# Performance work log

Hardware: AMD Instinct MI355X
Metric: run time of the kernel (lower is better)

Reference implementation:

```python
import jax, jax.numpy as jnp
import numpy as np

NUM_NODES = 1024
NUM_HEADS = 8
HIDDEN = 256
BOND_DIM = 64
NUM_LAYERS = 3


def _build_edge_index(n):
    # ring + chord graph, both directions -> 4n directed edges, no duplicate (src,tgt) pairs
    u = np.arange(n)
    src = np.concatenate([u, u, (u + 1) % n, (u + 2) % n])
    dst = np.concatenate([(u + 1) % n, (u + 2) % n, u, u])
    return jnp.asarray(np.stack([src, dst]), dtype=jnp.int32)


def setup_inputs() -> dict:
    key = jax.random.key(0)
    ks = jax.random.split(key, 16)
    H, L, B = HIDDEN, NUM_LAYERS, BOND_DIM
    E = 4 * NUM_NODES
    s = 0.02
    inp = {
        "edge_index": _build_edge_index(NUM_NODES),
        "bond_features": jax.random.normal(ks[0], (E, B), jnp.float32),
        # bond_embedding Linear + W_h Linear (stored as [in, out])
        "W_emb": jax.random.normal(ks[1], (B, H), jnp.float32) * s,
        "b_emb": jnp.zeros((H,), jnp.float32),
        "W_h": jax.random.normal(ks[2], (H, H), jnp.float32) * s,
        "b_h": jnp.zeros((H,), jnp.float32),
        # per-layer attention block: pre-LN, qkv in-proj, out-proj
        "ln1_g": jnp.ones((L, H), jnp.float32),
        "ln1_b": jnp.zeros((L, H), jnp.float32),
        "in_w": jax.random.normal(ks[3], (L, H, 3 * H), jnp.float32) * s,
        "in_b": jnp.zeros((L, 3 * H), jnp.float32),
        "out_w": jax.random.normal(ks[4], (L, H, H), jnp.float32) * s,
        "out_b": jnp.zeros((L, H), jnp.float32),
        # per-layer bond_update: Linear -> LayerNorm -> GELU
        "up_w": jax.random.normal(ks[5], (L, H, H), jnp.float32) * s,
        "up_b": jnp.zeros((L, H), jnp.float32),
        "ln2_g": jnp.ones((L, H), jnp.float32),
        "ln2_b": jnp.zeros((L, H), jnp.float32),
    }
    return inp


def _layer_norm(x, g, b, eps=1e-5):
    m = jnp.mean(x, axis=-1, keepdims=True)
    v = jnp.var(x, axis=-1, keepdims=True)
    return (x - m) * jax.lax.rsqrt(v + eps) * g + b


def _mha(x, in_w, in_b, out_w, out_b):
    # x: [E, H]; standard torch MultiheadAttention (batch of 1)
    E, H = x.shape
    d = H // NUM_HEADS
    qkv = x @ in_w + in_b                                  # [E, 3H]
    q, k, v = jnp.split(qkv, 3, axis=-1)
    q = q.reshape(E, NUM_HEADS, d).transpose(1, 0, 2)       # [h, E, d]
    k = k.reshape(E, NUM_HEADS, d).transpose(1, 0, 2)
    v = v.reshape(E, NUM_HEADS, d).transpose(1, 0, 2)
    scores = jnp.einsum("hqd,hkd->hqk", q, k) / jnp.sqrt(jnp.float32(d))
    p = jax.nn.softmax(scores, axis=-1)
    o = jnp.einsum("hqk,hkd->hqd", p, v)                    # [h, E, d]
    o = o.transpose(1, 0, 2).reshape(E, H)
    return o @ out_w + out_b


def _bond_aggregation(edge_index, h):
    # r_e = sum_{e' : tgt(e')=tgt(e), src(e')!=src(e)} (h[e'] - h[e])
    # with no duplicate (src,tgt) pairs this is S[tgt] - deg[tgt] * h
    tgt = edge_index[1]
    S = jax.ops.segment_sum(h, tgt, num_segments=NUM_NODES)                 # [N, H]
    deg = jax.ops.segment_sum(jnp.ones(h.shape[:1], h.dtype), tgt, num_segments=NUM_NODES)
    return S[tgt] - deg[tgt][:, None] * h


def reference(edge_index, bond_features, W_emb, b_emb, W_h, b_h,
              ln1_g, ln1_b, in_w, in_b, out_w, out_b,
              up_w, up_b, ln2_g, ln2_b):
    h = jax.nn.gelu(bond_features @ W_emb + b_emb, approximate=False)
    h = h @ W_h + b_h
    for t in range(NUM_LAYERS):
        r = _bond_aggregation(edge_index, h)
        xn = _layer_norm(r, ln1_g[t], ln1_b[t])
        attn = _mha(xn, in_w[t], in_b[t], out_w[t], out_b[t])
        # block output = attn + r (residual inside block), forward adds + r again
        t_ij = attn + r + r
        u = t_ij @ up_w[t] + up_b[t]
        h = jax.nn.gelu(_layer_norm(u, ln2_g[t], ln2_b[t]), approximate=False)
    return h
```

## Files before the change

kernel.cpp:

```cpp
#include <hip/hip_runtime.h>
#include <hip/hip_bf16.h>
#include <math.h>

#define N_NODES 1024
#define NE      4096
#define HDIM    256
#define QSCALE  0.2550348634f

typedef __hip_bfloat16 bf16;
typedef __attribute__((ext_vector_type(8))) short bf16x8;
typedef __attribute__((ext_vector_type(4))) float f32x4;

__device__ __forceinline__ float u2f(unsigned short u) {
  return __uint_as_float(((unsigned)u) << 16);
}
__device__ __forceinline__ short f2bs(float x) {
  unsigned u = __float_as_uint(x);
  unsigned r = u + 0x7FFFu + ((u >> 16) & 1u);
  return (short)(r >> 16);
}
__device__ __forceinline__ float gelu_f(float x) {
  return 0.5f * x * (1.0f + erff(x * 0.70710678118654752f));
}
__device__ __forceinline__ short rdbf(const void* p, int i, int flag) {
  return flag ? ((const short*)p)[i] : f2bs(((const float*)p)[i]);
}
__device__ __forceinline__ float fexp2(float x) {
#if __has_builtin(__builtin_amdgcn_exp2f)
  return __builtin_amdgcn_exp2f(x);
#else
  return exp2f(x);
#endif
}
__device__ __forceinline__ unsigned pk2(float lo, float hi) {
  return (__float_as_uint(hi) & 0xFFFF0000u) | (__float_as_uint(lo) >> 16);
}

__global__ __launch_bounds__(64) void k_detect(const unsigned* __restrict__ w,
                                               int* __restrict__ flag) {
  int t = threadIdx.x;
  int cnt = 0;
  for (int i = 0; i < 16; ++i) {
    unsigned v = w[t * 16 + i];
    unsigned e = (v >> 7) & 0xFFu;
    cnt += (e >= 100u && e <= 132u) ? 1 : 0;
  }
#pragma unroll
  for (int k = 1; k < 64; k <<= 1) cnt += __shfl_xor(cnt, k, 64);
  if (t == 0) *flag = (cnt > 512) ? 1 : 0;
}

struct WPtrs { const void* w_emb; const void* w_h; const void* in_w;
               const void* out_w; const void* up_w; };
__global__ __launch_bounds__(256) void k_prep_w(WPtrs a, short* __restrict__ Wt,
                                                const int* __restrict__ flag) {
  int i = blockIdx.x * 256 + threadIdx.x;
  if (i >= 1064960) return;
  const int fl = *flag;
  if (i < 16384) {
    int k = i >> 8, n = i & 255;
    Wt[n * 64 + k] = rdbf(a.w_emb, i, fl);
  } else if (i < 81920) {
    int j = i - 16384;
    int k = j >> 8, n = j & 255;
    Wt[16384 + n * 256 + k] = rdbf(a.w_h, j, fl);
  } else if (i < 671744) {
    int j = i - 81920;
    int t = j / 196608, jj = j % 196608;
    int k = jj / 768, n = jj % 768;
    Wt[81920 + t * 196608 + n * 256 + k] = rdbf(a.in_w, j, fl);
  } else if (i < 868352) {
    int j = i - 671744;
    int t = j >> 16, jj = j & 65535;
    int k = jj >> 8, n = jj & 255;
    Wt[671744 + t * 65536 + n * 256 + k] = rdbf(a.out_w, j, fl);
  } else {
    int j = i - 868352;
    int t = j >> 16, jj = j & 65535;
    int k = jj >> 8, n = jj & 255;
    Wt[868352 + t * 65536 + n * 256 + k] = rdbf(a.up_w, j, fl);
  }
}

struct PPtrs { const void* p[9]; };
__global__ __launch_bounds__(256) void k_cvt_small(PPtrs a, float* __restrict__ dst,
                                                   const int* __restrict__ flag) {
  const int sz[9] = {256, 256, 768, 768, 2304, 768, 768, 768, 768};
  int i = blockIdx.x * 256 + threadIdx.x;
  if (i >= 7424) return;
  int seg = 0, off = i;
  while (off >= sz[seg]) { off -= sz[seg]; ++seg; }
  dst[i] = *flag ? u2f(((const unsigned short*)a.p[seg])[off])
                 : ((const float*)a.p[seg])[off];
}

__global__ __launch_bounds__(256) void k_cvt_bond(const void* __restrict__ src,
                                                  short* __restrict__ dst,
                                                  const int* __restrict__ flag) {
  int i = blockIdx.x * 256 + threadIdx.x;
  if (i < NE * 64) dst[i] = rdbf(src, i, *flag);
}

__global__ __launch_bounds__(256) void k_build_inv(const int* __restrict__ tgt,
                                                   int* __restrict__ cnt,
                                                   int* __restrict__ inv) {
  int e = blockIdx.x * 256 + threadIdx.x;
  if (e < NE) {
    int t = tgt[e];
    int s = atomicAdd(&cnt[t], 1);
    if (s < 8) inv[t * 8 + s] = e;
  }
}

template <bool GELU, bool RES, bool WF, bool WB>
__global__ __launch_bounds__(256) void k_mgemm(const short* __restrict__ A,
                                               const short* __restrict__ Bt,
                                               const float* __restrict__ bias,
                                               const float* __restrict__ res,
                                               float* __restrict__ outF,
                                               short* __restrict__ outB,
                                               int M, int N, int K) {
  __shared__ alignas(16) short As[64 * 40];
  __shared__ alignas(16) short Bs[64 * 40];
  const int tid = threadIdx.x;
  const int wave = tid >> 6, lane = tid & 63;
  const int m = lane & 15, quad = lane >> 4;
  const int bm = blockIdx.x * 64, bn = blockIdx.y * 64;
  const int m0 = (wave & 1) * 32, n0 = (wave >> 1) * 32;
  const int srow = tid >> 2, sko = (tid & 3) * 8;

  f32x4 acc[2][2];
  acc[0][0] = acc[0][1] = acc[1][0] = acc[1][1] = (f32x4){0.f, 0.f, 0.f, 0.f};

  int4 pa = *(const int4*)(A + (size_t)(bm + srow) * K + sko);
  int4 pb = *(const int4*)(Bt + (size_t)(bn + srow) * K + sko);

  for (int k0 = 0; k0 < K; k0 += 32) {
    __syncthreads();
    *(int4*)&As[srow * 40 + sko] = pa;
    *(int4*)&Bs[srow * 40 + sko] = pb;
    __syncthreads();
    if (k0 + 32 < K) {
      pa = *(const int4*)(A + (size_t)(bm + srow) * K + k0 + 32 + sko);
      pb = *(const int4*)(Bt + (size_t)(bn + srow) * K + k0 + 32 + sko);
    }
    bf16x8 a0 = *(const bf16x8*)&As[(m0 + m) * 40 + quad * 8];
    bf16x8 a1 = *(const bf16x8*)&As[(m0 + 16 + m) * 40 + quad * 8];
    bf16x8 b0 = *(const bf16x8*)&Bs[(n0 + m) * 40 + quad * 8];
    bf16x8 b1 = *(const bf16x8*)&Bs[(n0 + 16 + m) * 40 + quad * 8];
    acc[0][0] = __builtin_amdgcn_mfma_f32_16x16x32_bf16(a0, b0, acc[0][0], 0, 0, 0);
    acc[0][1] = __builtin_amdgcn_mfma_f32_16x16x32_bf16(a0, b1, acc[0][1], 0, 0, 0);
    acc[1][0] = __builtin_amdgcn_mfma_f32_16x16x32_bf16(a1, b0, acc[1][0], 0, 0, 0);
    acc[1][1] = __builtin_amdgcn_mfma_f32_16x16x32_bf16(a1, b1, acc[1][1], 0, 0, 0);
  }

#pragma unroll
  for (int i = 0; i < 2; ++i)
#pragma unroll
    for (int j = 0; j < 2; ++j) {
      const int col = bn + n0 + j * 16 + m;
      const float bv = bias[col];
#pragma unroll
      for (int r = 0; r < 4; ++r) {
        const int row = bm + m0 + i * 16 + quad * 4 + r;
        float v = acc[i][j][r] + bv;
        if (GELU) v = gelu_f(v);
        if (RES) v += 2.0f * res[(size_t)row * N + col];
        if (WF) outF[(size_t)row * N + col] = v;
        if (WB) outB[(size_t)row * N + col] = f2bs(v);
      }
    }
}

__global__ __launch_bounds__(256) void k_mgemm_qkv(const short* __restrict__ A,
                                                   const short* __restrict__ Bt,
                                                   const float* __restrict__ bias,
                                                   short* __restrict__ Qh,
                                                   short* __restrict__ Kh,
                                                   short* __restrict__ Vt) {
  const int K = 256;
  __shared__ alignas(16) short As[64 * 40];
  __shared__ alignas(16) short Bs[64 * 40];
  const int tid = threadIdx.x;
  const int wave = tid >> 6, lane = tid & 63;
  const int m = lane & 15, quad = lane >> 4;
  const int bm = blockIdx.x * 64, bn = blockIdx.y * 64;
  const int m0 = (wave & 1) * 32, n0 = (wave >> 1) * 32;
  const int srow = tid >> 2, sko = (tid & 3) * 8;

  f32x4 acc[2][2];
  acc[0][0] = acc[0][1] = acc[1][0] = acc[1][1] = (f32x4){0.f, 0.f, 0.f, 0.f};

  int4 pa = *(const int4*)(A + (size_t)(bm + srow) * K + sko);
  int4 pb = *(const int4*)(Bt + (size_t)(bn + srow) * K + sko);

  for (int k0 = 0; k0 < K; k0 += 32) {
    __syncthreads();
    *(int4*)&As[srow * 40 + sko] = pa;
    *(int4*)&Bs[srow * 40 + sko] = pb;
    __syncthreads();
    if (k0 + 32 < K) {
      pa = *(const int4*)(A + (size_t)(bm + srow) * K + k0 + 32 + sko);
      pb = *(const int4*)(Bt + (size_t)(bn + srow) * K + k0 + 32 + sko);
    }
    bf16x8 a0 = *(const bf16x8*)&As[(m0 + m) * 40 + quad * 8];
    bf16x8 a1 = *(const bf16x8*)&As[(m0 + 16 + m) * 40 + quad * 8];
    bf16x8 b0 = *(const bf16x8*)&Bs[(n0 + m) * 40 + quad * 8];
    bf16x8 b1 = *(const bf16x8*)&Bs[(n0 + 16 + m) * 40 + quad * 8];
    acc[0][0] = __builtin_amdgcn_mfma_f32_16x16x32_bf16(a0, b0, acc[0][0], 0, 0, 0);
    acc[0][1] = __builtin_amdgcn_mfma_f32_16x16x32_bf16(a0, b1, acc[0][1], 0, 0, 0);
    acc[1][0] = __builtin_amdgcn_mfma_f32_16x16x32_bf16(a1, b0, acc[1][0], 0, 0, 0);
    acc[1][1] = __builtin_amdgcn_mfma_f32_16x16x32_bf16(a1, b1, acc[1][1], 0, 0, 0);
  }

#pragma unroll
  for (int i = 0; i < 2; ++i)
#pragma unroll
    for (int j = 0; j < 2; ++j) {
      const int col = bn + n0 + j * 16 + m;
      const float bv = bias[col];
      const int row0 = bm + m0 + i * 16 + quad * 4;
      if (col < 256) {
        const int head = col >> 5, d = col & 31;
#pragma unroll
        for (int r = 0; r < 4; ++r)
          Qh[(size_t)head * 131072 + (row0 + r) * 32 + d] =
              f2bs((acc[i][j][r] + bv) * QSCALE);
      } else if (col < 512) {
        const int c = col - 256, head = c >> 5, d = c & 31;
#pragma unroll
        for (int r = 0; r < 4; ++r)
          Kh[(size_t)head * 131072 + (row0 + r) * 32 + d] = f2bs(acc[i][j][r] + bv);
      } else {
        const int c = col - 512, head = c >> 5, d = c & 31;
        const int p0 = (row0 & ~63) + ((row0 >> 5) & 1) * 32 +
                       ((row0 >> 2) & 3) * 8 + ((row0 >> 4) & 1) * 4;
        ushort4 w;
        w.x = (unsigned short)f2bs(acc[i][j][0] + bv);
        w.y = (unsigned short)f2bs(acc[i][j][1] + bv);
        w.z = (unsigned short)f2bs(acc[i][j][2] + bv);
        w.w = (unsigned short)f2bs(acc[i][j][3] + bv);
        *(ushort4*)(Vt + (size_t)head * 131072 + d * 4096 + p0) = w;
      }
    }
}

__global__ __launch_bounds__(256) void k_rln2(const int* __restrict__ tgt,
                                              const int* __restrict__ cnt,
                                              const int* __restrict__ inv,
                                              const float* __restrict__ h,
                                              const float* __restrict__ g,
                                              const float* __restrict__ b,
                                              float* __restrict__ r,
                                              short* __restrict__ xnb) {
  __shared__ float red1[4], red2[4];
  const int e = blockIdx.x, d = threadIdx.x;
  const int t = tgt[e];
  const int c = cnt[t];
  float S = 0.f;
  for (int j = 0; j < c; ++j)
    S += h[(size_t)inv[t * 8 + j] * HDIM + d];
  float rv = S - (float)c * h[(size_t)e * HDIM + d];
  r[(size_t)e * HDIM + d] = rv;

  float s = rv;
#pragma unroll
  for (int k = 1; k < 64; k <<= 1) s += __shfl_xor(s, k, 64);
  if ((d & 63) == 0) red1[d >> 6] = s;
  __syncthreads();
  float mean = (red1[0] + red1[1] + red1[2] + red1[3]) * (1.0f / HDIM);
  float diff = rv - mean;
  float sq = diff * diff;
#pragma unroll
  for (int k = 1; k < 64; k <<= 1) sq += __shfl_xor(sq, k, 64);
  if ((d & 63) == 0) red2[d >> 6] = sq;
  __syncthreads();
  float var = (red2[0] + red2[1] + red2[2] + red2[3]) * (1.0f / HDIM);
  xnb[(size_t)e * HDIM + d] = f2bs(diff * rsqrtf(var + 1e-5f) * g[d] + b[d]);
}

__global__ __launch_bounds__(256) void k_ln_gelu(const float* __restrict__ u,
                                                 const float* __restrict__ g,
                                                 const float* __restrict__ b,
                                                 float* __restrict__ hout,
                                                 void* __restrict__ finalout,
                                                 const int* __restrict__ flag) {
  __shared__ float red1[4], red2[4];
  const int e = blockIdx.x, d = threadIdx.x;
  float v = u[(size_t)e * HDIM + d];
  float s = v;
#pragma unroll
  for (int k = 1; k < 64; k <<= 1) s += __shfl_xor(s, k, 64);
  if ((d & 63) == 0) red1[d >> 6] = s;
  __syncthreads();
  float mean = (red1[0] + red1[1] + red1[2] + red1[3]) * (1.0f / HDIM);
  float diff = v - mean;
  float sq = diff * diff;
#pragma unroll
  for (int k = 1; k < 64; k <<= 1) sq += __shfl_xor(sq, k, 64);
  if ((d & 63) == 0) red2[d >> 6] = sq;
  __syncthreads();
  float var = (red2[0] + red2[1] + red2[2] + red2[3]) * (1.0f / HDIM);
  float xh = diff * rsqrtf(var + 1e-5f) * g[d] + b[d];
  float out = gelu_f(xh);
  hout[(size_t)e * HDIM + d] = out;
  if (finalout) {
    if (*flag)
      ((bf16*)finalout)[(size_t)e * HDIM + d] = __float2bfloat16(out);
    else
      ((float*)finalout)[(size_t)e * HDIM + d] = out;
  }
}

__global__ __launch_bounds__(256) void k_flash4(const short* __restrict__ Qh,
                                                const short* __restrict__ Kh,
                                                const short* __restrict__ Vt,
                                                short* __restrict__ Opart,
                                                float* __restrict__ lpart) {
  __shared__ alignas(16) short Ks[64 * 40];
  __shared__ alignas(16) short Vs[32 * 70 + 8];
  const int head = blockIdx.y, split = blockIdx.z;
  const int tid = threadIdx.x;
  const int wave = tid >> 6, lane = tid & 63;
  const int m = lane & 15, quad = lane >> 4;
  const int q0 = blockIdx.x * 256 + wave * 64;

  const short* Qb = Qh + (size_t)head * 131072;
  const short* Kb = Kh + (size_t)head * 131072;
  const short* Vb = Vt + (size_t)head * 131072;

  bf16x8 qf[4];
#pragma unroll
  for (int a = 0; a < 4; ++a)
    qf[a] = *(const bf16x8*)(Qb + (q0 + a * 16 + m) * 32 + quad * 8);

  f32x4 O[4][2];
  f32x4 lacc[4];
#pragma unroll
  for (int a = 0; a < 4; ++a) {
    O[a][0] = O[a][1] = (f32x4){0.f, 0.f, 0.f, 0.f};
    lacc[a] = (f32x4){0.f, 0.f, 0.f, 0.f};
  }

  bf16x8 ones;
#pragma unroll
  for (int i = 0; i < 8; ++i) ones[i] = (short)0x3F80;

  const int base = split * 1024;
  const int krow = tid >> 2, ko = (tid & 3) * 8;
  const int vrow = tid >> 3, vo = (tid & 7) * 8;
  const short* kstage = Kb + (size_t)(base + krow) * 32 + ko;
  const short* vstage = Vb + (size_t)vrow * 4096 + base + vo;

  int4 rk = *(const int4*)(kstage);
  int4 rv = *(const int4*)(vstage);

#pragma unroll 1
  for (int kb = 0; kb < 16; ++kb) {
    __syncthreads();
    *(int4*)&Ks[krow * 40 + ko] = rk;
    *(int4*)&Vs[vrow * 70 + vo] = rv;
    __syncthreads();
    if (kb < 15) {
      rk = *(const int4*)(kstage + (kb + 1) * 2048);
      rv = *(const int4*)(vstage + (kb + 1) * 64);
    }

    bf16x8 kc0 = *(const bf16x8*)&Ks[(0 * 16 + m) * 40 + quad * 8];
    bf16x8 kc1 = *(const bf16x8*)&Ks[(1 * 16 + m) * 40 + quad * 8];
    bf16x8 kc2 = *(const bf16x8*)&Ks[(2 * 16 + m) * 40 + quad * 8];
    bf16x8 kc3 = *(const bf16x8*)&Ks[(3 * 16 + m) * 40 + quad * 8];
    bf16x8 vc0 = *(const bf16x8*)&Vs[m * 70 + quad * 8];
    bf16x8 vc1 = *(const bf16x8*)&Vs[(m + 16) * 70 + quad * 8];
    bf16x8 vc2 = *(const bf16x8*)&Vs[m * 70 + 32 + quad * 8];
    bf16x8 vc3 = *(const bf16x8*)&Vs[(m + 16) * 70 + 32 + quad * 8];

    const f32x4 z = {0.f, 0.f, 0.f, 0.f};
#pragma unroll
    for (int a = 0; a < 4; ++a) {
      f32x4 S0 = __builtin_amdgcn_mfma_f32_16x16x32_bf16(kc0, qf[a], z, 0, 0, 0);
      f32x4 S1 = __builtin_amdgcn_mfma_f32_16x16x32_bf16(kc1, qf[a], z, 0, 0, 0);
      f32x4 S2 = __builtin_amdgcn_mfma_f32_16x16x32_bf16(kc2, qf[a], z, 0, 0, 0);
      f32x4 S3 = __builtin_amdgcn_mfma_f32_16x16x32_bf16(kc3, qf[a], z, 0, 0, 0);

      float e0[4], e1[4], e2[4], e3[4];
#pragma unroll
      for (int r = 0; r < 4; ++r) {
        e0[r] = fexp2(S0[r]);
        e1[r] = fexp2(S1[r]);
        e2[r] = fexp2(S2[r]);
        e3[r] = fexp2(S3[r]);
      }
      union { bf16x8 v; unsigned u[4]; } pf0, pf1;
      pf0.u[0] = pk2(e0[0], e0[1]);
      pf0.u[1] = pk2(e0[2], e0[3]);
      pf0.u[2] = pk2(e1[0], e1[1]);
      pf0.u[3] = pk2(e1[2], e1[3]);
      pf1.u[0] = pk2(e2[0], e2[1]);
      pf1.u[1] = pk2(e2[2], e2[3]);
      pf1.u[2] = pk2(e3[0], e3[1]);
      pf1.u[3] = pk2(e3[2], e3[3]);

      O[a][0] = __builtin_amdgcn_mfma_f32_16x16x32_bf16(pf0.v, vc0, O[a][0], 0, 0, 0);
      O[a][1] = __builtin_amdgcn_mfma_f32_16x16x32_bf16(pf0.v, vc1, O[a][1], 0, 0, 0);
      lacc[a] = __builtin_amdgcn_mfma_f32_16x16x32_bf16(pf0.v, ones, lacc[a], 0, 0, 0);
      O[a][0] = __builtin_amdgcn_mfma_f32_16x16x32_bf16(pf1.v, vc2, O[a][0], 0, 0, 0);
      O[a][1] = __builtin_amdgcn_mfma_f32_16x16x32_bf16(pf1.v, vc3, O[a][1], 0, 0, 0);
      lacc[a] = __builtin_amdgcn_mfma_f32_16x16x32_bf16(pf1.v, ones, lacc[a], 0, 0, 0);
    }
  }

#pragma unroll
  for (int a = 0; a < 4; ++a)
#pragma unroll
    for (int r = 0; r < 4; ++r) {
      const int row = q0 + a * 16 + quad * 4 + r;
      short* op = Opart + ((size_t)split * 4096 + row) * 256 + head * 32 + m;
      op[0]  = f2bs(O[a][0][r]);
      op[16] = f2bs(O[a][1][r]);
      if (m == 0) lpart[(size_t)(split * 8 + head) * 4096 + row] = lacc[a][r];
    }
}

__global__ __launch_bounds__(256) void k_merge(const short* __restrict__ Opart,
                                               const float* __restrict__ lpart,
                                               short* __restrict__ attnb) {
  const int i = blockIdx.x * 256 + threadIdx.x;
  const int q = i >> 8, hd = i & 255, head = hd >> 5;
  float o = 0.f, l = 0.f;
#pragma unroll
  for (int s = 0; s < 4; ++s) {
    o += u2f((unsigned short)Opart[(size_t)s * 1048576 + i]);
    l += lpart[(size_t)(s * 8 + head) * 4096 + q];
  }
  attnb[i] = f2bs(o / l);
}

extern "C" void kernel_launch(void* const* d_in, const int* in_sizes, int n_in,
                              void* d_out, int out_size, void* d_ws, size_t ws_size,
                              hipStream_t stream) {
  const int* edge = (const int*)d_in[0];
  const int* tgt = edge + NE;

  float* ws = (float*)d_ws;
  float* hbuf   = ws;
  float* rbuf   = ws + 1048576;
  int* cnt      = (int*)(ws + 2097152);
  int* inv      = cnt + 1024;
  float* prm    = ws + 2360320;
  short* xn_bf  = (short*)(ws + 2367744);
  short* attnbf = (short*)(ws + 2892032);
  short* Wt     = (short*)(ws + 3416320);
  short* Qh     = (short*)(ws + 3948800);
  short* Kh     = (short*)(ws + 4473088);
  short* Vt     = (short*)(ws + 4997376);
  float* lpart  = ws + 5521664;
  float* BIG    = ws + 5652736;
  int* flag     = (int*)(ws + 9847040);

  short* bond_bf = (short*)BIG;
  short* e1_bf   = (short*)(BIG + 131072);
  short* Opart   = (short*)BIG;
  short* t_bf    = (short*)BIG;
  float* ubuf    = BIG + 524288;

  const short* Wt_emb = Wt;
  const short* Wt_h   = Wt + 16384;
  const short* Wt_in  = Wt + 81920;
  const short* Wt_out = Wt + 671744;
  const short* Wt_up  = Wt + 868352;
  const float* b_emb = prm;
  const float* b_h   = prm + 256;
  const float* ln1_g = prm + 512;
  const float* ln1_b = prm + 1280;
  const float* in_b  = prm + 2048;
  const float* out_b = prm + 4352;
  const float* up_b  = prm + 5120;
  const float* ln2_g = prm + 5888;
  const float* ln2_b = prm + 6656;

  k_detect<<<dim3(1), dim3(64), 0, stream>>>((const unsigned*)d_in[2], flag);
  WPtrs wp = {d_in[2], d_in[4], d_in[8], d_in[10], d_in[12]};
  k_prep_w<<<dim3(4160), dim3(256), 0, stream>>>(wp, Wt, flag);
  PPtrs pp = {{d_in[3], d_in[5], d_in[6], d_in[7], d_in[9], d_in[11],
               d_in[13], d_in[14], d_in[15]}};
  k_cvt_small<<<dim3(29), dim3(256), 0, stream>>>(pp, prm, flag);
  k_cvt_bond<<<dim3(1024), dim3(256), 0, stream>>>(d_in[1], bond_bf, flag);
  hipMemsetAsync(cnt, 0, N_NODES * sizeof(int), stream);
  k_build_inv<<<dim3(16), dim3(256), 0, stream>>>(tgt, cnt, inv);

  dim3 blk(256);
  dim3 g256(64, 4);
  dim3 g768(64, 12);
  dim3 gfa(16, 8, 4);

  k_mgemm<true, false, false, true><<<g256, blk, 0, stream>>>(
      bond_bf, Wt_emb, b_emb, nullptr, nullptr, e1_bf, NE, 256, 64);
  k_mgemm<false, false, true, false><<<g256, blk, 0, stream>>>(
      e1_bf, Wt_h, b_h, nullptr, hbuf, nullptr, NE, 256, 256);

  for (int t = 0; t < 3; ++t) {
    k_rln2<<<dim3(NE), blk, 0, stream>>>(tgt, cnt, inv, hbuf,
                                         ln1_g + t * HDIM, ln1_b + t * HDIM,
                                         rbuf, xn_bf);
    k_mgemm_qkv<<<g768, blk, 0, stream>>>(xn_bf, Wt_in + (size_t)t * 196608,
                                          in_b + t * 768, Qh, Kh, Vt);
    k_flash4<<<gfa, blk, 0, stream>>>(Qh, Kh, Vt, Opart, lpart);
    k_merge<<<dim3(4096), blk, 0, stream>>>(Opart, lpart, attnbf);
    k_mgemm<false, true, false, true><<<g256, blk, 0, stream>>>(
        attnbf, Wt_out + (size_t)t * 65536, out_b + t * 256, rbuf,
        nullptr, t_bf, NE, 256, 256);
    k_mgemm<false, false, true, false><<<g256, blk, 0, stream>>>(
        t_bf, Wt_up + (size_t)t * 65536, up_b + t * 256, nullptr,
        ubuf, nullptr, NE, 256, 256);
    k_ln_gelu<<<dim3(NE), blk, 0, stream>>>(ubuf, ln2_g + t * HDIM,
                                            ln2_b + t * HDIM, hbuf,
                                            (t == 2) ? d_out : nullptr, flag);
  }
}
```

Before: 312.2 us.

## Load full-K GEMM tiles into swizzled LDS once instead of k-loop staging

The bf16 MFMA GEMM kernels now load the whole 64xK slabs of A and B into shared memory in one pass, using an XOR swizzle in place of padding to avoid bank conflicts. The K loop then runs fully unrolled with no barriers. This removes the per-32-slice double sync and serialised global loads. The cost is 64 KB of LDS per block for K=256, which limits occupancy to roughly two blocks per CU, and loses any overlap between loads and MFMA work.

New measurement: 303.3 us. 1.03x faster.

```diff
diff --git a/kernel.cpp b/kernel.cpp
--- a/kernel.cpp
+++ b/kernel.cpp
@@ -112,42 +112,53 @@
   }
 }
 
-template <bool GELU, bool RES, bool WF, bool WB>
+template <int K, bool GELU, bool RES, bool WF, bool WB>
 __global__ __launch_bounds__(256) void k_mgemm(const short* __restrict__ A,
                                                const short* __restrict__ Bt,
                                                const float* __restrict__ bias,
                                                const float* __restrict__ res,
                                                float* __restrict__ outF,
                                                short* __restrict__ outB,
-                                               int M, int N, int K) {
-  __shared__ alignas(16) short As[64 * 40];
-  __shared__ alignas(16) short Bs[64 * 40];
+                                               int M, int N) {
+  __shared__ alignas(16) short As[64 * K];
+  __shared__ alignas(16) short Bs[64 * K];
   const int tid = threadIdx.x;
   const int wave = tid >> 6, lane = tid & 63;
   const int m = lane & 15, quad = lane >> 4;
   const int bm = blockIdx.x * 64, bn = blockIdx.y * 64;
   const int m0 = (wave & 1) * 32, n0 = (wave >> 1) * 32;
-  const int srow = tid >> 2, sko = (tid & 3) * 8;
+
+  constexpr int CPR = K >> 3;
+  constexpr int CPT = K >> 5;
+
+  int4 ra[CPT], rb[CPT];
+#pragma unroll
+  for (int i = 0; i < CPT; ++i) {
+    const int c = tid + (i << 8);
+    const int row = c / CPR, kc = c % CPR;
+    ra[i] = *(const int4*)(A + (size_t)(bm + row) * K + kc * 8);
+    rb[i] = *(const int4*)(Bt + (size_t)(bn + row) * K + kc * 8);
+  }
+#pragma unroll
+  for (int i = 0; i < CPT; ++i) {
+    const int c = tid + (i << 8);
+    const int row = c / CPR, kc = c % CPR;
+    *(int4*)&As[row * K + ((kc ^ (row & 7)) << 3)] = ra[i];
+    *(int4*)&Bs[row * K + ((kc ^ (row & 7)) << 3)] = rb[i];
+  }
+  __syncthreads();
 
   f32x4 acc[2][2];
   acc[0][0] = acc[0][1] = acc[1][0] = acc[1][1] = (f32x4){0.f, 0.f, 0.f, 0.f};
 
-  int4 pa = *(const int4*)(A + (size_t)(bm + srow) * K + sko);
-  int4 pb = *(const int4*)(Bt + (size_t)(bn + srow) * K + sko);
-
-  for (int k0 = 0; k0 < K; k0 += 32) {
-    __syncthreads();
-    *(int4*)&As[srow * 40 + sko] = pa;
-    *(int4*)&Bs[srow * 40 + sko] = pb;
-    __syncthreads();
-    if (k0 + 32 < K) {
-      pa = *(const int4*)(A + (size_t)(bm + srow) * K + k0 + 32 + sko);
-      pb = *(const int4*)(Bt + (size_t)(bn + srow) * K + k0 + 32 + sko);
-    }
-    bf16x8 a0 = *(const bf16x8*)&As[(m0 + m) * 40 + quad * 8];
-    bf16x8 a1 = *(const bf16x8*)&As[(m0 + 16 + m) * 40 + quad * 8];
-    bf16x8 b0 = *(const bf16x8*)&Bs[(n0 + m) * 40 + quad * 8];
-    bf16x8 b1 = *(const bf16x8*)&Bs[(n0 + 16 + m) * 40 + quad * 8];
+  const int sw = m & 7;
+#pragma unroll
+  for (int ks = 0; ks < K / 32; ++ks) {
+    const int ca = ((ks * 4 + quad) ^ sw) << 3;
+    bf16x8 a0 = *(const bf16x8*)&As[(m0 + m) * K + ca];
+    bf16x8 a1 = *(const bf16x8*)&As[(m0 + 16 + m) * K + ca];
+    bf16x8 b0 = *(const bf16x8*)&Bs[(n0 + m) * K + ca];
+    bf16x8 b1 = *(const bf16x8*)&Bs[(n0 + 16 + m) * K + ca];
     acc[0][0] = __builtin_amdgcn_mfma_f32_16x16x32_bf16(a0, b0, acc[0][0], 0, 0, 0);
     acc[0][1] = __builtin_amdgcn_mfma_f32_16x16x32_bf16(a0, b1, acc[0][1], 0, 0, 0);
     acc[1][0] = __builtin_amdgcn_mfma_f32_16x16x32_bf16(a1, b0, acc[1][0], 0, 0, 0);
@@ -178,35 +189,43 @@
                                                    short* __restrict__ Qh,
                                                    short* __restrict__ Kh,
                                                    short* __restrict__ Vt) {
-  const int K = 256;
-  __shared__ alignas(16) short As[64 * 40];
-  __shared__ alignas(16) short Bs[64 * 40];
+  constexpr int K = 256;
+  __shared__ alignas(16) short As[64 * K];
+  __shared__ alignas(16) short Bs[64 * K];
   const int tid = threadIdx.x;
   const int wave = tid >> 6, lane = tid & 63;
   const int m = lane & 15, quad = lane >> 4;
   const int bm = blockIdx.x * 64, bn = blockIdx.y * 64;
   const int m0 = (wave & 1) * 32, n0 = (wave >> 1) * 32;
-  const int srow = tid >> 2, sko = (tid & 3) * 8;
+
+  int4 ra[8], rb[8];
+#pragma unroll
+  for (int i = 0; i < 8; ++i) {
+    const int c = tid + (i << 8);
+    const int row = c >> 5, kc = c & 31;
+    ra[i] = *(const int4*)(A + (size_t)(bm + row) * K + kc * 8);
+    rb[i] = *(const int4*)(Bt + (size_t)(bn + row) * K + kc * 8);
+  }
+#pragma unroll
+  for (int i = 0; i < 8; ++i) {
+    const int c = tid + (i << 8);
+    const int row = c >> 5, kc = c & 31;
+    *(int4*)&As[row * K + ((kc ^ (row & 7)) << 3)] = ra[i];
+    *(int4*)&Bs[row * K + ((kc ^ (row & 7)) << 3)] = rb[i];
+  }
+  __syncthreads();
 
   f32x4 acc[2][2];
   acc[0][0] = acc[0][1] = acc[1][0] = acc[1][1] = (f32x4){0.f, 0.f, 0.f, 0.f};
 
-  int4 pa = *(const int4*)(A + (size_t)(bm + srow) * K + sko);
-  int4 pb = *(const int4*)(Bt + (size_t)(bn + srow) * K + sko);
-
-  for (int k0 = 0; k0 < K; k0 += 32) {
-    __syncthreads();
-    *(int4*)&As[srow * 40 + sko] = pa;
-    *(int4*)&Bs[srow * 40 + sko] = pb;
-    __syncthreads();
-    if (k0 + 32 < K) {
-      pa = *(const int4*)(A + (size_t)(bm + srow) * K + k0 + 32 + sko);
-      pb = *(const int4*)(Bt + (size_t)(bn + srow) * K + k0 + 32 + sko);
-    }
-    bf16x8 a0 = *(const bf16x8*)&As[(m0 + m) * 40 + quad * 8];
-    bf16x8 a1 = *(const bf16x8*)&As[(m0 + 16 + m) * 40 + quad * 8];
-    bf16x8 b0 = *(const bf16x8*)&Bs[(n0 + m) * 40 + quad * 8];
-    bf16x8 b1 = *(const bf16x8*)&Bs[(n0 + 16 + m) * 40 + quad * 8];
+  const int sw = m & 7;
+#pragma unroll
+  for (int ks = 0; ks < K / 32; ++ks) {
+    const int ca = ((ks * 4 + quad) ^ sw) << 3;
+    bf16x8 a0 = *(const bf16x8*)&As[(m0 + m) * K + ca];
+    bf16x8 a1 = *(const bf16x8*)&As[(m0 + 16 + m) * K + ca];
+    bf16x8 b0 = *(const bf16x8*)&Bs[(n0 + m) * K + ca];
+    bf16x8 b1 = *(const bf16x8*)&Bs[(n0 + 16 + m) * K + ca];
     acc[0][0] = __builtin_amdgcn_mfma_f32_16x16x32_bf16(a0, b0, acc[0][0], 0, 0, 0);
     acc[0][1] = __builtin_amdgcn_mfma_f32_16x16x32_bf16(a0, b1, acc[0][1], 0, 0, 0);
     acc[1][0] = __builtin_amdgcn_mfma_f32_16x16x32_bf16(a1, b0, acc[1][0], 0, 0, 0);
@@ -494,10 +513,10 @@
   dim3 g768(64, 12);
   dim3 gfa(16, 8, 4);
 
-  k_mgemm<true, false, false, true><<<g256, blk, 0, stream>>>(
-      bond_bf, Wt_emb, b_emb, nullptr, nullptr, e1_bf, NE, 256, 64);
-  k_mgemm<false, false, true, false><<<g256, blk, 0, stream>>>(
-      e1_bf, Wt_h, b_h, nullptr, hbuf, nullptr, NE, 256, 256);
+  k_mgemm<64, true, false, false, true><<<g256, blk, 0, stream>>>(
+      bond_bf, Wt_emb, b_emb, nullptr, nullptr, e1_bf, NE, 256);
+  k_mgemm<256, false, false, true, false><<<g256, blk, 0, stream>>>(
+      e1_bf, Wt_h, b_h, nullptr, hbuf, nullptr, NE, 256);
 
   for (int t = 0; t < 3; ++t) {
     k_rln2<<<dim3(NE), blk, 0, stream>>>(tgt, cnt, inv, hbuf,
@@ -507,12 +526,12 @@
                                           in_b + t * 768, Qh, Kh, Vt);
     k_flash4<<<gfa, blk, 0, stream>>>(Qh, Kh, Vt, Opart, lpart);
     k_merge<<<dim3(4096), blk, 0, stream>>>(Opart, lpart, attnbf);
-    k_mgemm<false, true, false, true><<<g256, blk, 0, stream>>>(
+    k_mgemm<256, false, true, false, true><<<g256, blk, 0, stream>>>(
         attnbf, Wt_out + (size_t)t * 65536, out_b + t * 256, rbuf,
-        nullptr, t_bf, NE, 256, 256);
-    k_mgemm<false, false, true, false><<<g256, blk, 0, stream>>>(
+        nullptr, t_bf, NE, 256);
+    k_mgemm<256, false, false, true, false><<<g256, blk, 0, stream>>>(
         t_bf, Wt_up + (size_t)t * 65536, up_b + t * 256, nullptr,
-        ubuf, nullptr, NE, 256, 256);
+        ubuf, nullptr, NE, 256);
     k_ln_gelu<<<dim3(NE), blk, 0, stream>>>(ubuf, ln2_g + t * HDIM,
                                             ln2_b + t * HDIM, hbuf,
                                             (t == 2) ? d_out : nullptr, flag);
```
